# Kernel optimization log

Hardware: AMD Instinct MI355X
Metric: run time of the kernel (lower is better)

Reference implementation:

```python
import jax, jax.numpy as jnp
import numpy as np


def setup_inputs() -> dict:
    key = jax.random.key(0)
    k1, k2 = jax.random.split(key)
    B, D, T = 8, 64, 8192
    K = 1024
    z = jax.random.normal(k1, (B, D, T), dtype=jnp.float32)
    # nn.init.uniform_(-1/K, 1/K)
    codebook = jax.random.uniform(k2, (K, D), dtype=jnp.float32,
                                  minval=-1.0 / K, maxval=1.0 / K)
    return {"z": z, "codebook": codebook}


def reference(z, codebook):
    # z: [B, D, T], codebook: [K, D]
    z_t = jnp.transpose(z, (0, 2, 1))  # [B, T, D]
    # squared L2 distances: ||z||^2 + ||e||^2 - 2 z.e  -> [B, T, K]
    d = (jnp.sum(z_t * z_t, axis=-1, keepdims=True)
         + jnp.sum(codebook * codebook, axis=-1)
         - 2.0 * jnp.einsum('btd,kd->btk', z_t, codebook))
    codes = jnp.argmin(d, axis=-1)  # [B, T] int
    quantized = jnp.transpose(codebook[codes], (0, 2, 1))  # [B, D, T]
    # straight-through estimator
    quantized_st = z + jax.lax.stop_gradient(quantized - z)
    commit_loss = jnp.mean((jax.lax.stop_gradient(quantized) - z) ** 2)
    return codes, quantized_st, commit_loss
```

## Files before the change

### kernel.cpp

```cpp
#include <hip/hip_runtime.h>
#include <hip/hip_bf16.h>

typedef __attribute__((ext_vector_type(8))) short short8;
typedef __attribute__((ext_vector_type(4))) float f32x4;

constexpr int Bb = 8;
constexpr int Dd = 64;
constexpr int Tt = 8192;
constexpr int Kk = 1024;
constexpr int BT = Bb * Tt;
constexpr int NTOT = Bb * Dd * Tt;

constexpr int OUT_Q_OFF = BT;
constexpr int OUT_LOSS_OFF = BT + NTOT;

constexpr size_t WS_CODES_OFF = 0;
constexpr size_t WS_PREC_OFF  = (size_t)BT * 4;
constexpr size_t WS_PART_OFF  = WS_PREC_OFF + 4096;
constexpr size_t WS_EH_OFF    = WS_PART_OFF + 4096;
constexpr size_t WS_EM_OFF    = WS_EH_OFF + (size_t)Kk * Dd * 2;
constexpr size_t WS_EL_OFF    = WS_EM_OFF + (size_t)Kk * Dd * 2;

__device__ inline ushort rne_bf16(float v) {
    unsigned u = __float_as_uint(v);
    return (ushort)((u + 0x7FFFu + ((u >> 16) & 1u)) >> 16);
}
__device__ inline float bf16f(ushort h) { return __uint_as_float(((unsigned)h) << 16); }

__global__ void __launch_bounds__(256) prep_kernel(const float* __restrict__ cb,
                                                   float* __restrict__ prec,
                                                   ushort* __restrict__ eh,
                                                   ushort* __restrict__ em,
                                                   ushort* __restrict__ el) {
    const int k = blockIdx.x * 256 + threadIdx.x;
    const float4* row = reinterpret_cast<const float4*>(cb + (size_t)k * Dd);
    float4 v[16];
    float s = 0.f;
#pragma unroll
    for (int i = 0; i < 16; ++i) {
        v[i] = row[i];
        s = fmaf(v[i].x, v[i].x, s); s = fmaf(v[i].y, v[i].y, s);
        s = fmaf(v[i].z, v[i].z, s); s = fmaf(v[i].w, v[i].w, s);
    }
    prec[k] = s;
#pragma unroll
    for (int g = 0; g < 8; ++g) {
        float vals[8] = {v[2*g].x, v[2*g].y, v[2*g].z, v[2*g].w,
                         v[2*g+1].x, v[2*g+1].y, v[2*g+1].z, v[2*g+1].w};
        short8 hv, mv, lv;
#pragma unroll
        for (int j = 0; j < 8; ++j) {
            float x = vals[j];
            ushort h = rne_bf16(x);  float hf = bf16f(h);
            float r1 = x - hf;       ushort m = rne_bf16(r1); float mf = bf16f(m);
            float r2 = r1 - mf;      ushort l = rne_bf16(r2);
            hv[j] = (short)h; mv[j] = (short)m; lv[j] = (short)l;
        }
        const size_t base = (size_t)k * 64 + g * 8;
        *reinterpret_cast<short8*>(eh + base) = hv;
        *reinterpret_cast<short8*>(em + base) = mv;
        *reinterpret_cast<short8*>(el + base) = lv;
    }
}

constexpr int TM = 64;
constexpr int NKT = Kk / 64;

__global__ void __launch_bounds__(256, 2) mfma_argmin_kernel(
    const float* __restrict__ z,
    const ushort* __restrict__ eh, const ushort* __restrict__ em,
    const ushort* __restrict__ el,
    const float* __restrict__ prec, float* __restrict__ out,
    int* __restrict__ codes_i)
{
    __shared__ __align__(16) ushort z_lds[3 * 64 * 64];
    __shared__ float zsq_part[4][64];
    __shared__ float zsq_lds[64];
    __shared__ float red_v[4][64];
    __shared__ int   red_i[4][64];

    const int tid = threadIdx.x;
    const int lane = tid & 63;
    const int w = tid >> 6;
    const int row0 = blockIdx.x * TM;
    const int b = row0 >> 13;
    const int t0 = row0 & (Tt - 1);

    {
        const int tt = tid & 63;
        const int dg = tid >> 6;
        const float* zp = z + (size_t)b * (Dd * Tt) + (size_t)(dg * 16) * Tt + (t0 + tt);
        float vals[16];
        float psum = 0.f;
#pragma unroll
        for (int i = 0; i < 16; ++i) {
            float v = zp[(size_t)i * Tt];
            vals[i] = v;
            psum = fmaf(v, v, psum);
        }
        zsq_part[dg][tt] = psum;
#pragma unroll
        for (int g = 0; g < 2; ++g) {
            short8 hv, mv, lv;
#pragma unroll
            for (int j = 0; j < 8; ++j) {
                float v = vals[g * 8 + j];
                ushort h = rne_bf16(v);  float hf = bf16f(h);
                float r1 = v - hf;       ushort m = rne_bf16(r1); float mf = bf16f(m);
                float r2 = r1 - mf;      ushort l = rne_bf16(r2);
                hv[j] = (short)h; mv[j] = (short)m; lv[j] = (short)l;
            }
            const int byte_in_row = dg * 32 + g * 16;
            const int sw = tt * 128 + (byte_in_row ^ ((tt & 7) << 4));
            *reinterpret_cast<short8*>((char*)z_lds + 0 * 8192 + sw) = hv;
            *reinterpret_cast<short8*>((char*)z_lds + 1 * 8192 + sw) = mv;
            *reinterpret_cast<short8*>((char*)z_lds + 2 * 8192 + sw) = lv;
        }
    }
    __syncthreads();
    if (tid < 64)
        zsq_lds[tid] = ((zsq_part[0][tid] + zsq_part[1][tid]) + zsq_part[2][tid]) + zsq_part[3][tid];
    __syncthreads();

    short8 A[3][2][4];
#pragma unroll
    for (int sA = 0; sA < 3; ++sA)
#pragma unroll
        for (int ds = 0; ds < 2; ++ds)
#pragma unroll
            for (int rf = 0; rf < 4; ++rf) {
                const int row = rf * 16 + (lane & 15);
                const int dby = ds * 64 + ((lane >> 4) * 16);
                A[sA][ds][rf] = *reinterpret_cast<const short8*>(
                    (char*)z_lds + sA * 8192 + row * 128 + (dby ^ ((row & 7) << 4)));
            }

    float zsq_r[16];
#pragma unroll
    for (int rf = 0; rf < 4; ++rf)
#pragma unroll
        for (int j = 0; j < 4; ++j)
            zsq_r[rf * 4 + j] = zsq_lds[rf * 16 + (lane >> 4) * 4 + j];

    float bestv[16];
    int   besti[16];
#pragma unroll
    for (int i = 0; i < 16; ++i) { bestv[i] = 3.4e38f; besti[i] = 0; }

    const int kl = lane & 15;
    const int d0 = (lane >> 4) * 8;

#define LOAD_B(Bx, esqx, KT)                                                    \
    {                                                                           \
        const size_t kg = (size_t)((KT) * 64 + w * 16 + kl);                    \
        const size_t base = kg * 64 + d0;                                       \
        Bx[0] = *reinterpret_cast<const short8*>(eh + base);                    \
        Bx[1] = *reinterpret_cast<const short8*>(eh + base + 32);               \
        Bx[2] = *reinterpret_cast<const short8*>(em + base);                    \
        Bx[3] = *reinterpret_cast<const short8*>(em + base + 32);               \
        Bx[4] = *reinterpret_cast<const short8*>(el + base);                    \
        Bx[5] = *reinterpret_cast<const short8*>(el + base + 32);               \
        esqx = prec[kg];                                                        \
    }

#define TILE_STEP(Bx, esqx, KT)                                                 \
    {                                                                           \
        f32x4 acc[4];                                                           \
        _Pragma("unroll")                                                       \
        for (int rf = 0; rf < 4; ++rf) acc[rf] = (f32x4){0.f, 0.f, 0.f, 0.f};   \
        _Pragma("unroll")                                                       \
        for (int ds = 0; ds < 2; ++ds) {                                        \
            _Pragma("unroll")                                                   \
            for (int rf = 0; rf < 4; ++rf)                                      \
                acc[rf] = __builtin_amdgcn_mfma_f32_16x16x32_bf16(A[0][ds][rf], Bx[0 * 2 + ds], acc[rf], 0, 0, 0); \
            _Pragma("unroll")                                                   \
            for (int rf = 0; rf < 4; ++rf)                                      \
                acc[rf] = __builtin_amdgcn_mfma_f32_16x16x32_bf16(A[0][ds][rf], Bx[1 * 2 + ds], acc[rf], 0, 0, 0); \
            _Pragma("unroll")                                                   \
            for (int rf = 0; rf < 4; ++rf)                                      \
                acc[rf] = __builtin_amdgcn_mfma_f32_16x16x32_bf16(A[0][ds][rf], Bx[2 * 2 + ds], acc[rf], 0, 0, 0); \
            _Pragma("unroll")                                                   \
            for (int rf = 0; rf < 4; ++rf)                                      \
                acc[rf] = __builtin_amdgcn_mfma_f32_16x16x32_bf16(A[1][ds][rf], Bx[0 * 2 + ds], acc[rf], 0, 0, 0); \
            _Pragma("unroll")                                                   \
            for (int rf = 0; rf < 4; ++rf)                                      \
                acc[rf] = __builtin_amdgcn_mfma_f32_16x16x32_bf16(A[1][ds][rf], Bx[1 * 2 + ds], acc[rf], 0, 0, 0); \
            _Pragma("unroll")                                                   \
            for (int rf = 0; rf < 4; ++rf)                                      \
                acc[rf] = __builtin_amdgcn_mfma_f32_16x16x32_bf16(A[2][ds][rf], Bx[0 * 2 + ds], acc[rf], 0, 0, 0); \
        }                                                                       \
        const int kglob = (KT) * 64 + w * 16 + kl;                              \
        _Pragma("unroll")                                                       \
        for (int rf = 0; rf < 4; ++rf)                                          \
            _Pragma("unroll")                                                   \
            for (int j = 0; j < 4; ++j) {                                       \
                const float t1 = zsq_r[rf * 4 + j] + esqx;                      \
                const float s = fmaf(-2.f, acc[rf][j], t1);                     \
                if (s < bestv[rf * 4 + j]) { bestv[rf * 4 + j] = s; besti[rf * 4 + j] = kglob; } \
            }                                                                   \
    }

    short8 B0[6], B1[6];
    float esq0, esq1;
    LOAD_B(B0, esq0, 0)
    LOAD_B(B1, esq1, 1)

    for (int kt = 0; kt < NKT; kt += 2) {
        TILE_STEP(B0, esq0, kt)
        if (kt + 2 < NKT) LOAD_B(B0, esq0, kt + 2)
        TILE_STEP(B1, esq1, kt + 1)
        if (kt + 3 < NKT) LOAD_B(B1, esq1, kt + 3)
    }
#undef LOAD_B
#undef TILE_STEP

#pragma unroll
    for (int i = 0; i < 16; ++i) {
#pragma unroll
        for (int m = 1; m < 16; m <<= 1) {
            const float ov = __shfl_xor(bestv[i], m, 16);
            const int   oi = __shfl_xor(besti[i], m, 16);
            if (ov < bestv[i] || (ov == bestv[i] && oi < besti[i])) {
                bestv[i] = ov; besti[i] = oi;
            }
        }
    }
    if ((lane & 15) == 0) {
#pragma unroll
        for (int rf = 0; rf < 4; ++rf)
#pragma unroll
            for (int j = 0; j < 4; ++j) {
                const int row = rf * 16 + (lane >> 4) * 4 + j;
                red_v[w][row] = bestv[rf * 4 + j];
                red_i[w][row] = besti[rf * 4 + j];
            }
    }
    __syncthreads();
    if (tid < 64) {
        float bv = red_v[0][tid];
        int   bi = red_i[0][tid];
#pragma unroll
        for (int s2 = 1; s2 < 4; ++s2) {
            const float v = red_v[s2][tid];
            const int   i = red_i[s2][tid];
            if (v < bv || (v == bv && i < bi)) { bv = v; bi = i; }
        }
        codes_i[row0 + tid] = bi;
        out[row0 + tid] = (float)bi;
    }
}

__global__ void __launch_bounds__(256) quant_kernel(
    const float* __restrict__ z, const float* __restrict__ cb,
    const int* __restrict__ codes_i, float* __restrict__ out,
    float* __restrict__ partials)
{
    const int row = blockIdx.x * 256 + threadIdx.x;
    const int b = row >> 13;
    const int t = row & (Tt - 1);
    const int code = codes_i[row];
    const float4* crow = reinterpret_cast<const float4*>(cb + (size_t)code * Dd);
    const float* zbase = z + (size_t)b * (Dd * Tt) + t;
    float* obase = out + OUT_Q_OFF + (size_t)b * (Dd * Tt) + t;

    float acc = 0.f;
#pragma unroll
    for (int d4 = 0; d4 < 16; ++d4) {
        float4 v = crow[d4];
        float vv[4] = {v.x, v.y, v.z, v.w};
#pragma unroll
        for (int j = 0; j < 4; ++j) {
            const int d = d4 * 4 + j;
            const float zv = zbase[(size_t)d * Tt];
            const float diff = vv[j] - zv;
            acc = fmaf(diff, diff, acc);
            obase[(size_t)d * Tt] = vv[j];
        }
    }

    __shared__ float red[256];
    red[threadIdx.x] = acc;
    __syncthreads();
#pragma unroll
    for (int s = 128; s > 0; s >>= 1) {
        if (threadIdx.x < s) red[threadIdx.x] += red[threadIdx.x + s];
        __syncthreads();
    }
    if (threadIdx.x == 0) partials[blockIdx.x] = red[0];
}

__global__ void __launch_bounds__(256) loss_kernel(const float* __restrict__ partials,
                                                   float* __restrict__ out) {
    __shared__ float red[256];
    red[threadIdx.x] = partials[threadIdx.x];
    __syncthreads();
#pragma unroll
    for (int s = 128; s > 0; s >>= 1) {
        if (threadIdx.x < s) red[threadIdx.x] += red[threadIdx.x + s];
        __syncthreads();
    }
    if (threadIdx.x == 0)
        out[OUT_LOSS_OFF] = red[0] * (1.0f / (float)NTOT);
}

extern "C" void kernel_launch(void* const* d_in, const int* in_sizes, int n_in,
                              void* d_out, int out_size, void* d_ws, size_t ws_size,
                              hipStream_t stream) {
    const float* z = (const float*)d_in[0];
    const float* cb = (const float*)d_in[1];
    float* out = (float*)d_out;

    char* ws = (char*)d_ws;
    int* codes_i = (int*)(ws + WS_CODES_OFF);
    float* prec = (float*)(ws + WS_PREC_OFF);
    float* partials = (float*)(ws + WS_PART_OFF);
    ushort* eh = (ushort*)(ws + WS_EH_OFF);
    ushort* em = (ushort*)(ws + WS_EM_OFF);
    ushort* el = (ushort*)(ws + WS_EL_OFF);

    prep_kernel<<<Kk / 256, 256, 0, stream>>>(cb, prec, eh, em, el);
    mfma_argmin_kernel<<<BT / TM, 256, 0, stream>>>(z, eh, em, el, prec, out, codes_i);
    quant_kernel<<<BT / 256, 256, 0, stream>>>(z, cb, codes_i, out, partials);
    loss_kernel<<<1, 256, 0, stream>>>(partials, out);
}
```

Before: 91.85 us.

## Software-pipeline MFMA blocks with epilogue of previous tile using double accumulators

Splits the per-tile work into an MFMA block and an argmin epilogue, using two accumulator sets so the epilogue for tile k runs while the MFMAs for tile k+1 are in flight. It also reorders the MFMA chain by d-slice and starts from a zero operand instead of explicitly zeroing the accumulators. Loads are clamped to the last tile rather than guarded by a branch, so the final iterations issue redundant loads. This hides MFMA latency behind VALU compare work, at the cost of more accumulator registers, which could reduce occupancy.

```diff
diff --git a/kernel.cpp b/kernel.cpp
--- a/kernel.cpp
+++ b/kernel.cpp
@@ -163,56 +163,86 @@
         esqx = prec[kg];                                                        \
     }
 
-#define TILE_STEP(Bx, esqx, KT)                                                 \
+#define MFMA_BLOCK(accX, Bx)                                                    \
     {                                                                           \
-        f32x4 acc[4];                                                           \
-        _Pragma("unroll")                                                       \
-        for (int rf = 0; rf < 4; ++rf) acc[rf] = (f32x4){0.f, 0.f, 0.f, 0.f};   \
-        _Pragma("unroll")                                                       \
-        for (int ds = 0; ds < 2; ++ds) {                                        \
-            _Pragma("unroll")                                                   \
-            for (int rf = 0; rf < 4; ++rf)                                      \
-                acc[rf] = __builtin_amdgcn_mfma_f32_16x16x32_bf16(A[0][ds][rf], Bx[0 * 2 + ds], acc[rf], 0, 0, 0); \
-            _Pragma("unroll")                                                   \
-            for (int rf = 0; rf < 4; ++rf)                                      \
-                acc[rf] = __builtin_amdgcn_mfma_f32_16x16x32_bf16(A[0][ds][rf], Bx[1 * 2 + ds], acc[rf], 0, 0, 0); \
-            _Pragma("unroll")                                                   \
-            for (int rf = 0; rf < 4; ++rf)                                      \
-                acc[rf] = __builtin_amdgcn_mfma_f32_16x16x32_bf16(A[0][ds][rf], Bx[2 * 2 + ds], acc[rf], 0, 0, 0); \
-            _Pragma("unroll")                                                   \
-            for (int rf = 0; rf < 4; ++rf)                                      \
-                acc[rf] = __builtin_amdgcn_mfma_f32_16x16x32_bf16(A[1][ds][rf], Bx[0 * 2 + ds], acc[rf], 0, 0, 0); \
-            _Pragma("unroll")                                                   \
-            for (int rf = 0; rf < 4; ++rf)                                      \
-                acc[rf] = __builtin_amdgcn_mfma_f32_16x16x32_bf16(A[1][ds][rf], Bx[1 * 2 + ds], acc[rf], 0, 0, 0); \
-            _Pragma("unroll")                                                   \
-            for (int rf = 0; rf < 4; ++rf)                                      \
-                acc[rf] = __builtin_amdgcn_mfma_f32_16x16x32_bf16(A[2][ds][rf], Bx[0 * 2 + ds], acc[rf], 0, 0, 0); \
-        }                                                                       \
+        _Pragma("unroll")                                                       \
+        for (int rf = 0; rf < 4; ++rf)                                          \
+            accX[rf] = __builtin_amdgcn_mfma_f32_16x16x32_bf16(A[0][0][rf], Bx[0], (f32x4){0.f,0.f,0.f,0.f}, 0, 0, 0); \
+        _Pragma("unroll")                                                       \
+        for (int rf = 0; rf < 4; ++rf)                                          \
+            accX[rf] = __builtin_amdgcn_mfma_f32_16x16x32_bf16(A[0][0][rf], Bx[2], accX[rf], 0, 0, 0); \
+        _Pragma("unroll")                                                       \
+        for (int rf = 0; rf < 4; ++rf)                                          \
+            accX[rf] = __builtin_amdgcn_mfma_f32_16x16x32_bf16(A[0][0][rf], Bx[4], accX[rf], 0, 0, 0); \
+        _Pragma("unroll")                                                       \
+        for (int rf = 0; rf < 4; ++rf)                                          \
+            accX[rf] = __builtin_amdgcn_mfma_f32_16x16x32_bf16(A[1][0][rf], Bx[0], accX[rf], 0, 0, 0); \
+        _Pragma("unroll")                                                       \
+        for (int rf = 0; rf < 4; ++rf)                                          \
+            accX[rf] = __builtin_amdgcn_mfma_f32_16x16x32_bf16(A[1][0][rf], Bx[2], accX[rf], 0, 0, 0); \
+        _Pragma("unroll")                                                       \
+        for (int rf = 0; rf < 4; ++rf)                                          \
+            accX[rf] = __builtin_amdgcn_mfma_f32_16x16x32_bf16(A[2][0][rf], Bx[0], accX[rf], 0, 0, 0); \
+        _Pragma("unroll")                                                       \
+        for (int rf = 0; rf < 4; ++rf)                                          \
+            accX[rf] = __builtin_amdgcn_mfma_f32_16x16x32_bf16(A[0][1][rf], Bx[1], accX[rf], 0, 0, 0); \
+        _Pragma("unroll")                                                       \
+        for (int rf = 0; rf < 4; ++rf)                                          \
+            accX[rf] = __builtin_amdgcn_mfma_f32_16x16x32_bf16(A[0][1][rf], Bx[3], accX[rf], 0, 0, 0); \
+        _Pragma("unroll")                                                       \
+        for (int rf = 0; rf < 4; ++rf)                                          \
+            accX[rf] = __builtin_amdgcn_mfma_f32_16x16x32_bf16(A[0][1][rf], Bx[5], accX[rf], 0, 0, 0); \
+        _Pragma("unroll")                                                       \
+        for (int rf = 0; rf < 4; ++rf)                                          \
+            accX[rf] = __builtin_amdgcn_mfma_f32_16x16x32_bf16(A[1][1][rf], Bx[1], accX[rf], 0, 0, 0); \
+        _Pragma("unroll")                                                       \
+        for (int rf = 0; rf < 4; ++rf)                                          \
+            accX[rf] = __builtin_amdgcn_mfma_f32_16x16x32_bf16(A[1][1][rf], Bx[3], accX[rf], 0, 0, 0); \
+        _Pragma("unroll")                                                       \
+        for (int rf = 0; rf < 4; ++rf)                                          \
+            accX[rf] = __builtin_amdgcn_mfma_f32_16x16x32_bf16(A[2][1][rf], Bx[1], accX[rf], 0, 0, 0); \
+    }
+
+#define EPI(accX, esqx, KT)                                                     \
+    {                                                                           \
         const int kglob = (KT) * 64 + w * 16 + kl;                              \
         _Pragma("unroll")                                                       \
         for (int rf = 0; rf < 4; ++rf)                                          \
             _Pragma("unroll")                                                   \
             for (int j = 0; j < 4; ++j) {                                       \
                 const float t1 = zsq_r[rf * 4 + j] + esqx;                      \
-                const float s = fmaf(-2.f, acc[rf][j], t1);                     \
+                const float s = fmaf(-2.f, accX[rf][j], t1);                    \
                 if (s < bestv[rf * 4 + j]) { bestv[rf * 4 + j] = s; besti[rf * 4 + j] = kglob; } \
             }                                                                   \
     }
 
     short8 B0[6], B1[6];
     float esq0, esq1;
+    f32x4 accA[4], accB[4];
+
     LOAD_B(B0, esq0, 0)
     LOAD_B(B1, esq1, 1)
-
-    for (int kt = 0; kt < NKT; kt += 2) {
-        TILE_STEP(B0, esq0, kt)
-        if (kt + 2 < NKT) LOAD_B(B0, esq0, kt + 2)
-        TILE_STEP(B1, esq1, kt + 1)
-        if (kt + 3 < NKT) LOAD_B(B1, esq1, kt + 3)
-    }
+    MFMA_BLOCK(accA, B0)
+    float esqA = esq0;
+    LOAD_B(B0, esq0, 2)
+
+    for (int kt = 0; kt < NKT - 2; kt += 2) {
+        MFMA_BLOCK(accB, B1)
+        const float esqB = esq1;
+        EPI(accA, esqA, kt)
+        LOAD_B(B1, esq1, (kt + 3 < NKT - 1 ? kt + 3 : NKT - 1))
+        MFMA_BLOCK(accA, B0)
+        esqA = esq0;
+        EPI(accB, esqB, kt + 1)
+        LOAD_B(B0, esq0, (kt + 4 < NKT - 1 ? kt + 4 : NKT - 1))
+    }
+    MFMA_BLOCK(accB, B1)
+    EPI(accA, esqA, NKT - 2)
+    EPI(accB, esq1, NKT - 1)
+
 #undef LOAD_B
-#undef TILE_STEP
+#undef MFMA_BLOCK
+#undef EPI
 
 #pragma unroll
     for (int i = 0; i < 16; ++i) {
```

Result: slower. 93.94 us (+2.3%).
